# Performance work log

Hardware: AMD Instinct MI355X
Metric: run time of the kernel (lower is better)

The kernel has to match this reference:

```python
import math
import jax, jax.numpy as jnp
from jax import lax
import numpy as np

BSZ, NQ, L, DM, DI, H, HD, DDIST, DCONV, DHID = 2, 128, 2048, 256, 512, 8, 64, 16, 4, 64
DKEY = DI * 2 + 2 + H  # key_proj output: z + xbc + per-head dt bias
DCV = DI + 2           # depthwise conv channels


def setup_inputs() -> dict:
    key = jax.random.key(0)
    ks = jax.random.split(key, 40)
    it = iter(range(40))
    def n(shape, s=1.0):
        return jax.random.normal(ks[next(it)], shape, jnp.float32) * s
    # dt_bias init exactly as in torch module
    dt = jnp.exp(jax.random.uniform(ks[next(it)], (H,)) * (math.log(0.1) - math.log(0.001)) + math.log(0.001))
    dt = jnp.maximum(dt, 1e-4)
    dt_bias = dt + jnp.log(-jnp.expm1(-dt))
    A_log = jnp.log(jax.random.uniform(ks[next(it)], (H,), minval=1.0, maxval=16.0))
    return {
        'queries': n((BSZ, NQ, DM)), 'anchors': n((BSZ, NQ, 3), 10.0),
        'features_perm': n((BSZ, L, DM)), 'pos_embed_perm': n((BSZ, L, DM)),
        'key_pos_3d': n((BSZ, L, 3), 10.0), 'query_pos': n((BSZ, NQ, DM)),
        'key_proj_w': n((DM, DKEY), 0.02),
        'key_conv_w': n((DCV, DCONV), 0.1), 'key_conv_b': jnp.zeros((DCV,)),
        'query_proj_w': n((DM, DI), 0.02),
        'dist_w1': n((3, DHID), 0.3), 'dist_b1': jnp.zeros((DHID,)), 'dist_w2': n((DHID, DDIST), 0.1),
        'bc_proj_w': n((DDIST, 2), 0.2), 'dt_proj_w': n((DDIST, H), 0.2),
        'dt_bias': dt_bias, 'A_log': A_log, 'D': jnp.ones((H,)),
        'key_norm_w': jnp.ones((DI,)), 'out_key_proj_w': n((DI, DM), 0.02),
        'query_norm_w': jnp.ones((DI,)), 'query_norm_b': jnp.zeros((DI,)),
        'out_query_proj_w': n((DI, DM), 0.02),
        'ffn_norm_w': jnp.ones((DM,)), 'ffn_norm_b': jnp.zeros((DM,)),
        'ffn_fc1_w': n((DM, 8 * DM), 0.02), 'ffn_fc1_b': jnp.zeros((8 * DM,)),
        'ffn_fc2_w': n((4 * DM, DM), 0.02), 'ffn_fc2_b': jnp.zeros((DM,)),
    }


def _ln(x, w, b, eps=1e-5):
    m = jnp.mean(x, -1, keepdims=True)
    v = jnp.mean((x - m) ** 2, -1, keepdims=True)
    return (x - m) * lax.rsqrt(v + eps) * w + b


def _dwconv_causal(x, w, b):
    # x [B,L,C], w [C,K]; torch pads K-1 both sides then slices [:L] == causal left pad
    lhs = jnp.swapaxes(x, 1, 2)  # [B,C,L]
    out = lax.conv_general_dilated(lhs, w[:, None, :], (1,), [(DCONV - 1, 0)],
                                   feature_group_count=w.shape[0],
                                   dimension_numbers=('NCH', 'OIH', 'NCH'))
    return jnp.swapaxes(out + b[None, :, None], 1, 2)


def _issm(x, dt, A, Bs, Cs, Dp, init):
    # x [B,L,H,P]; dt [B,L,H,N]; A [H,N]; Bs/Cs [B,L,N]; init [B,H,P,N]
    def step(h, inp):
        xt, dtt, bt, ct = inp  # [B,H,P], [B,H,N], [B,N], [B,N]
        h = h * jnp.exp(dtt * A)[:, :, None, :] + (dtt * bt[:, None, :])[:, :, None, :] * xt[..., None]
        return h, jnp.einsum('bhpn,bn->bhp', h, ct)
    xs = (jnp.swapaxes(x, 0, 1), jnp.swapaxes(dt, 0, 1), jnp.swapaxes(Bs, 0, 1), jnp.swapaxes(Cs, 0, 1))
    h_last, ys = lax.scan(step, init, xs)
    y = jnp.swapaxes(ys, 0, 1) + x * Dp[None, None, :, None]  # D skip inside scan, as in ISSM_chunk_scan_combined
    return y, h_last


def _forward(queries, anchors, features_perm, pos_embed_perm, key_pos_3d, query_pos,
             key_proj_w, key_conv_w, key_conv_b, query_proj_w, dist_w1, dist_b1, dist_w2,
             bc_proj_w, dt_proj_w, dt_bias, A_log, D, key_norm_w, out_key_proj_w,
             query_norm_w, query_norm_b, out_query_proj_w, ffn_norm_w, ffn_norm_b,
             ffn_fc1_w, ffn_fc1_b, ffn_fc2_w, ffn_fc2_b):
    qp = queries + query_pos
    kp = (features_perm + pos_embed_perm) @ key_proj_w            # [B,L,DKEY]
    z, xbc, dtb_seq = kp[..., :DI], kp[..., DI:DI + DCV], kp[..., DI + DCV:]
    xbc = jax.nn.silu(_dwconv_causal(xbc, key_conv_w, key_conv_b))
    x = xbc[..., :DI]
    b_bias, c_bias = xbc[..., DI], xbc[..., DI + 1]               # [B,L]
    init = (qp @ query_proj_w).reshape(BSZ, NQ, H, HD).transpose(0, 2, 3, 1)  # [B,H,HD,NQ]
    # distance features: delta [B,L,NQ,3]
    delta = anchors[:, None, :, :] - key_pos_3d[:, :, None, :]
    enc = jnp.sign(delta) * jnp.log2(jnp.abs(delta) * 20.0 + 1.0) / math.log2(8.0) / 4.0
    feat = jax.nn.relu(enc @ dist_w1 + dist_b1) @ dist_w2         # [B,L,NQ,DDIST]
    bc = feat @ bc_proj_w                                         # [B,L,NQ,2]
    Bssm = bc[..., 0] + b_bias[..., None]                         # [B,L,NQ]
    Cssm = bc[..., 1] + c_bias[..., None]
    dtb = jnp.swapaxes(feat @ dt_proj_w, 2, 3)                    # [B,L,H,NQ]
    dt = jax.nn.softplus(dtb + dtb_seq[..., None] + dt_bias[None, None, :, None])
    A = jnp.broadcast_to(-jnp.exp(A_log)[:, None], (H, NQ))
    xs = x.reshape(BSZ, L, H, HD)
    y_f, h_f = _issm(xs, dt, A, Bssm, Cssm, D, init)
    fl = lambda a: jnp.flip(a, axis=1)
    y_b, h_b = _issm(fl(xs), fl(dt), A, fl(Bssm), fl(Cssm), D, init)
    y = (y_f + fl(y_b)) * 0.5
    h = (h_f + h_b) * 0.5                                         # [B,H,HD,NQ]
    y = y.reshape(BSZ, L, DI) + x * jnp.repeat(D, HD)[None, None, :]
    # gated RMSNorm (norm_before_gate=False): gate first, then normalize
    g = y * jax.nn.silu(z)
    g = g * lax.rsqrt(jnp.mean(g * g, -1, keepdims=True) + 1e-5) * key_norm_w
    out_feat = features_perm + g @ out_key_proj_w
    hs = h.transpose(0, 3, 1, 2).reshape(BSZ, NQ, DI)             # b h hd n -> b n (h hd)
    out_q = queries + _ln(hs, query_norm_w, query_norm_b) @ out_query_proj_w
    fn = _ln(out_q, ffn_norm_w, ffn_norm_b)
    a, v = jnp.split(fn @ ffn_fc1_w + ffn_fc1_b, 2, axis=-1)
    out_q = out_q + (jax.nn.gelu(a, approximate=False) * v) @ ffn_fc2_w + ffn_fc2_b
    return out_q, out_feat


def reference(queries, anchors, features_perm, pos_embed_perm, key_pos_3d, query_pos,
              key_proj_w, key_conv_w, key_conv_b, query_proj_w, dist_w1, dist_b1, dist_w2,
              bc_proj_w, dt_proj_w, dt_bias, A_log, D, key_norm_w, out_key_proj_w,
              query_norm_w, query_norm_b, out_query_proj_w, ffn_norm_w, ffn_norm_b,
              ffn_fc1_w, ffn_fc1_b, ffn_fc2_w, ffn_fc2_b):
    return _forward(queries, anchors, features_perm, pos_embed_perm, key_pos_3d, query_pos,
                    key_proj_w, key_conv_w, key_conv_b, query_proj_w, dist_w1, dist_b1, dist_w2,
                    bc_proj_w, dt_proj_w, dt_bias, A_log, D, key_norm_w, out_key_proj_w,
                    query_norm_w, query_norm_b, out_query_proj_w, ffn_norm_w, ffn_norm_b,
                    ffn_fc1_w, ffn_fc1_b, ffn_fc2_w, ffn_fc2_b)
```

## Files before the change

### kernel.cpp

```cpp
#include <hip/hip_runtime.h>

typedef unsigned short u16;
typedef __bf16 bf16x8 __attribute__((ext_vector_type(8)));
typedef u16 u16x8 __attribute__((ext_vector_type(8)));
typedef float f32x4 __attribute__((ext_vector_type(4)));

#define BSZ_ 2
#define NQ_ 128
#define LSEQ_ 2048
#define DM_ 256
#define DI_ 512
#define NH_ 8
#define HD_ 64
#define DKEY_ 1034
#define DCV_ 514
#define NCHUNK_ 16
#define CT_ 128

__device__ __forceinline__ float bf2f(u16 u) {
  unsigned v = ((unsigned)u) << 16;
  return __builtin_bit_cast(float, v);
}
__device__ __forceinline__ u16 f2bf(float f) {
  unsigned u = __builtin_bit_cast(unsigned, f);
  u += 0x7fffu + ((u >> 16) & 1u);
  return (u16)(u >> 16);
}
__device__ __forceinline__ float sigmoidf_(float x) { return 1.f / (1.f + expf(-x)); }
__device__ __forceinline__ float softplusf_(float x) {
  return (x > 20.f) ? x : log1pf(expf(x));
}

template<bool F32>
__device__ __forceinline__ float ldi(const void* p, size_t i) {
  return F32 ? ((const float*)p)[i] : bf2f(((const u16*)p)[i]);
}
template<bool F32>
__device__ __forceinline__ void sto(void* p, size_t i, float v) {
  if (F32) ((float*)p)[i] = v;
  else ((u16*)p)[i] = f2bf(v);
}

__device__ __forceinline__ bool detect_f32(const void* feat) {
  int lane = threadIdx.x & 63;
  float a = fabsf(bf2f(((const u16*)feat)[2*lane]));
  bool plaus = (a > 1e-6f) && (a < 1e6f);
  unsigned long long m = __ballot(plaus);
  return __popcll(m) < 32;
}

constexpr size_t SZ_KP    = (size_t)BSZ_*LSEQ_*DKEY_;
constexpr size_t SZ_XACT  = (size_t)BSZ_*LSEQ_*DCV_;
constexpr size_t SZ_AW    = (size_t)BSZ_*NH_*LSEQ_*NQ_*2;
constexpr size_t SZ_CARR  = (size_t)BSZ_*LSEQ_*NQ_;
constexpr size_t SZ_QPROJ = (size_t)BSZ_*NQ_*DI_;
constexpr size_t SZ_YACC  = (size_t)BSZ_*LSEQ_*DI_;
constexpr size_t SZ_SEND  = (size_t)BSZ_*NH_*2*NCHUNK_*NQ_*HD_;
constexpr size_t SZ_PTOT  = (size_t)BSZ_*NH_*2*NCHUNK_*NQ_;
constexpr size_t SZ_H0    = SZ_SEND;
constexpr size_t SZ_HB    = (size_t)BSZ_*NH_*2*NQ_*HD_;
constexpr size_t SZ_GBUF  = (size_t)BSZ_*LSEQ_*DI_/2;
constexpr size_t SZ_OUTQF = (size_t)BSZ_*NQ_*DM_;
constexpr size_t SZ_WPREP = 2048;

constexpr size_t OFF_KP    = 0;
constexpr size_t OFF_XACT  = OFF_KP + SZ_KP;
constexpr size_t OFF_AW    = OFF_XACT + SZ_XACT;
constexpr size_t OFF_CARR  = OFF_AW + SZ_AW;
constexpr size_t OFF_QPROJ = OFF_CARR + SZ_CARR;
constexpr size_t OFF_YACC  = OFF_QPROJ + SZ_QPROJ;
constexpr size_t OFF_SEND  = OFF_YACC + SZ_YACC;
constexpr size_t OFF_PTOT  = OFF_SEND + SZ_SEND;
constexpr size_t OFF_H0    = OFF_PTOT + SZ_PTOT;
constexpr size_t OFF_HB    = OFF_H0 + SZ_H0;
constexpr size_t OFF_GBUF  = OFF_HB + SZ_HB;
constexpr size_t OFF_OUTQF = OFF_GBUF + SZ_GBUF;
constexpr size_t OFF_WPREP = OFF_OUTQF + SZ_OUTQF;
constexpr size_t WS_FLOATS = OFF_WPREP + SZ_WPREP;

constexpr size_t OFF_UG  = OFF_AW;
constexpr size_t OFF_LNQ = OFF_UG + (size_t)256*1024/2;
constexpr size_t OFF_LNF = OFF_LNQ + (size_t)256*512/2;

constexpr size_t OFF_ABUF = OFF_SEND;
constexpr size_t OFF_AQ   = OFF_ABUF + (size_t)4096*256/2;
constexpr size_t OFF_BKEY = OFF_AQ + (size_t)256*256/2;
constexpr size_t OFF_BQ   = OFF_BKEY + (size_t)(256*1034+1)/2 + 1;
constexpr size_t OFF_BOK  = OFF_SEND;
constexpr size_t OFF_BOQ  = OFF_BOK + (size_t)512*256/2;
constexpr size_t OFF_B1W  = OFF_BOQ + (size_t)512*256/2;
constexpr size_t OFF_B2W  = OFF_B1W + (size_t)256*2048/2;

template<bool F32>
__device__ void prep_body(const void* A_log, const void* dt_bias,
                          const void* w1, const void* b1, const void* w2,
                          const void* bcw, const void* dtw, float* wp) {
  int t = threadIdx.x;
  if (t < 8) {
    wp[t]     = -expf(ldi<F32>(A_log, t));
    wp[8 + t] = ldi<F32>(dt_bias, t);
  }
  if (t < 64) {
    wp[32 + t*4 + 0] = ldi<F32>(w1, 0*64 + t);
    wp[32 + t*4 + 1] = ldi<F32>(w1, 1*64 + t);
    wp[32 + t*4 + 2] = ldi<F32>(w1, 2*64 + t);
    wp[32 + t*4 + 3] = ldi<F32>(b1, t);
  }
  for (int i = t; i < 1024; i += 256) wp[288 + i] = ldi<F32>(w2, i);
  if (t < 32)  wp[1312 + t] = ldi<F32>(bcw, t);
  if (t < 128) wp[1344 + t] = ldi<F32>(dtw, t);
}

__device__ __forceinline__ void cast_job(bool F32, const void* s0, const void* s1_,
                                         u16* d, size_t n, size_t base, size_t stride) {
  for (size_t i = base; i < n; i += stride) {
    float v = F32 ? ((const float*)s0)[i] : bf2f(((const u16*)s0)[i]);
    if (s1_) v += F32 ? ((const float*)s1_)[i] : bf2f(((const u16*)s1_)[i]);
    d[i] = f2bf(v);
  }
}

__global__ __launch_bounds__(256) void setup_kernel(
    const void* feat, const void* pe, u16* abuf,
    const void* q, const void* qp, u16* aq,
    const void* kw, u16* bkey, const void* qw, u16* bq,
    const void* A_log, const void* dt_bias, const void* w1, const void* b1,
    const void* w2, const void* bcw, const void* dtw, float* wp,
    float* yacc, int* flag)
{
  int bx = blockIdx.x, tid = threadIdx.x;
  if (bx < 512) {
    size_t base = (size_t)bx * 4096 + tid;
#pragma unroll
    for (int k = 0; k < 16; ++k) yacc[base + (size_t)k*256] = 0.f;
    return;
  }
  bool F32 = detect_f32(feat);
  if (bx < 1024) {
    cast_job(F32, feat, pe, abuf, (size_t)4096*256,
             (size_t)(bx-512)*256 + tid, (size_t)512*256);
  } else if (bx < 1056) {
    cast_job(F32, q, qp, aq, (size_t)256*256,
             (size_t)(bx-1024)*256 + tid, (size_t)32*256);
  } else if (bx < 1184) {
    cast_job(F32, kw, nullptr, bkey, (size_t)256*1034,
             (size_t)(bx-1056)*256 + tid, (size_t)128*256);
  } else if (bx < 1248) {
    cast_job(F32, qw, nullptr, bq, (size_t)256*512,
             (size_t)(bx-1184)*256 + tid, (size_t)64*256);
  } else {
    if (tid == 0) *flag = F32 ? 1 : 0;
    if (F32) prep_body<true>(A_log, dt_bias, w1, b1, w2, bcw, dtw, wp);
    else     prep_body<false>(A_log, dt_bias, w1, b1, w2, bcw, dtw, wp);
  }
}

template<int A_MODE, int B_MODE, int OUT_EXT, int RES_EXT, int RES_F32, int BIAS, bool F32>
__device__ void gemm_body(int bm, int bn,
                          const void* A0, const void* A1, const void* Bw,
                          float* Cf, void* Cext, const void* ResE,
                          const float* ResF, const void* Bias,
                          int M, int N, int K) {
  __shared__ u16 As[64][40];
  __shared__ u16 Bs[64][42];
  int tid = threadIdx.x;
  int w = tid >> 6, lane = tid & 63;
  f32x4 acc[4];
#pragma unroll
  for (int j = 0; j < 4; ++j) acc[j] = (f32x4){0.f, 0.f, 0.f, 0.f};

  int arow = tid >> 2, aseg = (tid & 3) * 8;
  int bkl = tid >> 3, bns = (tid & 7) * 8;

  for (int k0 = 0; k0 < K; k0 += 32) {
    {
      size_t abase = (size_t)(bm + arow) * K + k0 + aseg;
      u16x8 tv;
      if (A_MODE == 0) {
#pragma unroll
        for (int i = 0; i < 8; ++i)
          tv[i] = f2bf(ldi<F32>(A0, abase + i) + ldi<F32>(A1, abase + i));
      } else {
        const u16* pa = (const u16*)A0 + abase;
#pragma unroll
        for (int i = 0; i < 8; ++i) tv[i] = pa[i];
      }
      *(u16x8*)&As[arow][aseg] = tv;
    }
    {
      size_t bbase = (size_t)(k0 + bkl) * N + bn + bns;
#pragma unroll
      for (int i = 0; i < 8; ++i) {
        u16 v;
        if (bn + bns + i < N) {
          if (B_MODE == 1) v = ((const u16*)Bw)[bbase + i];
          else             v = f2bf(ldi<F32>(Bw, bbase + i));
        } else v = (u16)0;
        Bs[bns + i][bkl] = v;
      }
    }
    __syncthreads();
    int mrow = w * 16 + (lane & 15);
    int kq = (lane >> 4) * 8;
    bf16x8 af = __builtin_bit_cast(bf16x8, *(const u16x8*)&As[mrow][kq]);
#pragma unroll
    for (int j = 0; j < 4; ++j) {
      bf16x8 bfv = __builtin_bit_cast(bf16x8, *(const u16x8*)&Bs[j*16 + (lane & 15)][kq]);
      acc[j] = __builtin_amdgcn_mfma_f32_16x16x32_bf16(af, bfv, acc[j], 0, 0, 0);
    }
    __syncthreads();
  }
  int col0 = lane & 15, rbase = (lane >> 4) * 4;
#pragma unroll
  for (int j = 0; j < 4; ++j) {
#pragma unroll
    for (int r = 0; r < 4; ++r) {
      int row = bm + w * 16 + rbase + r;
      int col = bn + j * 16 + col0;
      if (col < N) {
        size_t idx = (size_t)row * N + col;
        float v = acc[j][r];
        if (BIAS)    v += ldi<F32>(Bias, col);
        if (RES_EXT) v += ldi<F32>(ResE, idx);
        if (RES_F32) v += ResF[idx];
        if (OUT_EXT) sto<F32>(Cext, idx, v);
        else         Cf[idx] = v;
      }
    }
  }
}

__global__ __launch_bounds__(256) void kp_gemm_kernel(
    const u16* abuf, const u16* bkey, float* kp) {
  gemm_body<1,1,0,0,0,0,false>(blockIdx.x*64, blockIdx.y*64, abuf, nullptr, bkey,
                               kp, nullptr, nullptr, nullptr, nullptr,
                               4096, DKEY_, DM_);
}

template<bool F32>
__device__ void fc2_body(const u16* ug, const u16* b2w, void* out_q,
                         const float* outqf, const void* b2) {
  gemm_body<1,1,1,0,1,1,F32>((blockIdx.x&3)*64, (blockIdx.x>>2)*64, ug, nullptr,
                             b2w, nullptr, out_q, nullptr, outqf, b2,
                             BSZ_*NQ_, DM_, 1024);
}
__global__ __launch_bounds__(256) void fc2_kernel(
    const int* fl, const u16* ug, const u16* b2w, void* out_q,
    const float* outqf, const void* b2) {
  if (*fl) fc2_body<true>(ug, b2w, out_q, outqf, b2);
  else     fc2_body<false>(ug, b2w, out_q, outqf, b2);
}

template<bool F32>
__device__ void conv_body(const float* kp, const void* cw, const void* cb,
                          float* xact) {
  int row = blockIdx.x;
  int l = row & (LSEQ_ - 1);
  for (int ch = threadIdx.x; ch < DCV_; ch += 256) {
    float acc = ldi<F32>(cb, ch);
#pragma unroll
    for (int k = 0; k < 4; ++k) {
      int ll = l - 3 + k;
      if (ll >= 0)
        acc = fmaf(ldi<F32>(cw, ch*4 + k), kp[(size_t)(row - 3 + k)*DKEY_ + DI_ + ch], acc);
    }
    xact[(size_t)row*DCV_ + ch] = acc * sigmoidf_(acc);
  }
}
__global__ __launch_bounds__(256) void convqp_kernel(
    const int* fl, const float* kp, const void* cw, const void* cb, float* xact,
    const u16* aq, const u16* bq, float* qproj)
{
  int bx = blockIdx.x;
  if (bx < 4096) {
    if (*fl) conv_body<true>(kp, cw, cb, xact);
    else     conv_body<false>(kp, cw, cb, xact);
  } else {
    int i = bx - 4096;
    gemm_body<1,1,0,0,0,0,false>((i&3)*64, (i>>2)*64, aq, nullptr, bq,
                                 qproj, nullptr, nullptr, nullptr, nullptr,
                                 BSZ_*NQ_, DI_, DM_);
  }
}

template<bool F32>
__device__ void dist_body(const void* anchors, const void* key_pos,
                          const float* kp, const float* xact, const float* wp,
                          float* aw, float* carr) {
  int tid = threadIdx.x;
  int n = tid & 127;
  int idx = blockIdx.x;
  int b = idx >> 10;
  int l = ((idx & 1023) << 1) | (tid >> 7);
  size_t row = (size_t)b * LSEQ_ + l;

  float enc0, enc1, enc2;
  {
    float e[3];
#pragma unroll
    for (int d = 0; d < 3; ++d) {
      float delta = ldi<F32>(anchors, (b*NQ_ + n)*3 + d) - ldi<F32>(key_pos, row*3 + d);
      float s = delta < 0.f ? -1.f : 1.f;
      e[d] = s * log2f(fabsf(delta) * 20.f + 1.f) * (1.f/12.f);
    }
    enc0 = e[0]; enc1 = e[1]; enc2 = e[2];
  }
  float feat[16];
#pragma unroll
  for (int f = 0; f < 16; ++f) feat[f] = 0.f;
  for (int j = 0; j < 64; ++j) {
    float w0 = wp[32 + j*4], w1v = wp[33 + j*4], w2v = wp[34 + j*4], bb = wp[35 + j*4];
    float hj = fmaxf(fmaf(enc0, w0, fmaf(enc1, w1v, fmaf(enc2, w2v, bb))), 0.f);
#pragma unroll
    for (int f = 0; f < 16; ++f) feat[f] = fmaf(hj, wp[288 + j*16 + f], feat[f]);
  }
  float bc0 = 0.f, bc1 = 0.f;
#pragma unroll
  for (int f = 0; f < 16; ++f) {
    bc0 = fmaf(feat[f], wp[1312 + f*2], bc0);
    bc1 = fmaf(feat[f], wp[1313 + f*2], bc1);
  }
  float bb_ = xact[row*DCV_ + DI_];
  float cb_ = xact[row*DCV_ + DI_ + 1];
  float Bs = bc0 + bb_, Cs = bc1 + cb_;
  carr[row*NQ_ + n] = Cs;

  float dtb[8];
#pragma unroll
  for (int h = 0; h < 8; ++h) dtb[h] = 0.f;
#pragma unroll
  for (int f = 0; f < 16; ++f)
#pragma unroll
    for (int h = 0; h < 8; ++h) dtb[h] = fmaf(feat[f], wp[1344 + f*8 + h], dtb[h]);

#pragma unroll
  for (int h = 0; h < 8; ++h) {
    float xln = dtb[h] + kp[row*DKEY_ + (DI_*2 + 2) + h] + wp[8 + h];
    float dtv = softplusf_(xln);
    float a = expf(dtv * wp[h]);
    float wv = dtv * Bs;
    size_t o = (((size_t)(b*NH_ + h)*LSEQ_ + l)*NQ_ + n)*2;
    aw[o] = a;
    aw[o + 1] = wv;
  }
}
__global__ __launch_bounds__(256) void dist_kernel(
    const int* fl, const void* anchors, const void* key_pos, const float* kp,
    const float* xact, const float* wp, float* aw, float* carr) {
  if (*fl) dist_body<true>(anchors, key_pos, kp, xact, wp, aw, carr);
  else     dist_body<false>(anchors, key_pos, kp, xact, wp, aw, carr);
}

__global__ __launch_bounds__(256) void s1m_kernel(
    const float* __restrict__ aw, const float* __restrict__ xact,
    float* __restrict__ send, float* __restrict__ ptot)
{
  int tid = threadIdx.x;
  int hd = tid & 63;
  int w = __builtin_amdgcn_readfirstlane(tid >> 6);
  int ns = blockIdx.x, q = blockIdx.y, z = blockIdx.z;
  int h = z & 7, b = z >> 3;
  int n0 = __builtin_amdgcn_readfirstlane(ns*16 + w*4);

  float hf[4], hb[4], pr[4];
#pragma unroll
  for (int i = 0; i < 4; ++i) { hf[i] = 0.f; hb[i] = 0.f; pr[i] = 1.f; }

  size_t awbase = (size_t)z * LSEQ_ * (NQ_*2);
  int t = q*CT_;
  for (int s = 0; s < CT_; ++s, ++t) {
    const float* awt = aw + awbase + (size_t)t*(NQ_*2) + n0*2;
    float xv = xact[((size_t)(b*LSEQ_ + t))*DCV_ + (h << 6) + hd];
#pragma unroll
    for (int i = 0; i < 4; ++i) {
      float a = awt[2*i], wv = awt[2*i + 1];
      float wx = wv * xv;
      hf[i] = fmaf(hf[i], a, wx);
      hb[i] = fmaf(pr[i], wx, hb[i]);
      pr[i] *= a;
    }
  }
  size_t cbf = (size_t)((z*2 + 0)*NCHUNK_ + q);
  size_t cbb = (size_t)((z*2 + 1)*NCHUNK_ + (NCHUNK_ - 1 - q));
#pragma unroll
  for (int i = 0; i < 4; ++i) {
    send[cbf*(NQ_*HD_) + (size_t)(n0 + i)*HD_ + hd] = hf[i];
    send[cbb*(NQ_*HD_) + (size_t)(n0 + i)*HD_ + hd] = hb[i];
  }
  if (hd == 0) {
#pragma unroll
    for (int i = 0; i < 4; ++i) {
      ptot[cbf*NQ_ + n0 + i] = pr[i];
      ptot[cbb*NQ_ + n0 + i] = pr[i];
    }
  }
}

__global__ __launch_bounds__(256) void s2_kernel(
    const float* __restrict__ qproj, const float* __restrict__ ptot,
    const float* __restrict__ send, float* __restrict__ h0buf,
    float* __restrict__ hbuf)
{
  int g = blockIdx.x*256 + threadIdx.x;
  int hd = g & 63;
  int n = (g >> 6) & 127;
  int dir = (g >> 13) & 1;
  int h = (g >> 14) & 7;
  int b = g >> 17;
  float hcur = qproj[((size_t)(b*NQ_ + n))*DI_ + h*HD_ + hd];
  size_t base = (size_t)((b*NH_ + h)*2 + dir) * NCHUNK_;
  for (int q = 0; q < NCHUNK_; ++q) {
    size_t cb = base + q;
    h0buf[cb*(NQ_*HD_) + (size_t)n*HD_ + hd] = hcur;
    hcur = fmaf(hcur, ptot[cb*NQ_ + n], send[cb*(NQ_*HD_) + (size_t)n*HD_ + hd]);
  }
  hbuf[((size_t)((b*NH_ + h)*2 + dir))*(NQ_*HD_) + (size_t)n*HD_ + hd] = hcur;
}

template<bool F32>
__device__ void cast1_part(const void* okw, u16* bok, const void* oqw, u16* boq,
                           const void* w1, u16* b1w, const void* w2, u16* b2w) {
  int i = blockIdx.x - 2048;
  int job = i >> 7, bj = i & 127;
  size_t base = (size_t)bj*256 + threadIdx.x, stride = (size_t)128*256;
  switch (job) {
    case 0: cast_job(F32, okw, nullptr, bok, (size_t)512*256, base, stride); break;
    case 1: cast_job(F32, oqw, nullptr, boq, (size_t)512*256, base, stride); break;
    case 2: cast_job(F32, w1, nullptr, b1w, (size_t)256*2048, base, stride); break;
    default: cast_job(F32, w2, nullptr, b2w, (size_t)1024*256, base, stride); break;
  }
}
__global__ __launch_bounds__(256) void s3cast_kernel(
    const int* fl, const float* __restrict__ aw, const float* __restrict__ carr,
    const float* __restrict__ xact, const float* __restrict__ h0buf,
    float* __restrict__ yacc,
    const void* okw, u16* bok, const void* oqw, u16* boq,
    const void* w1, u16* b1w, const void* w2, u16* b2w)
{
  int bx = blockIdx.x;
  if (bx >= 2048) {
    if (*fl) cast1_part<true>(okw, bok, oqw, boq, w1, b1w, w2, b2w);
    else     cast1_part<false>(okw, bok, oqw, boq, w1, b1w, w2, b2w);
    return;
  }
  int tid = threadIdx.x;
  int hd = tid & 63;
  int w = __builtin_amdgcn_readfirstlane(tid >> 6);
  int ns = bx & 3, q = (bx >> 2) & 15, zz = bx >> 6;
  int dir = zz & 1, h = (zz >> 1) & 7, b = zz >> 4;
  int z = b*NH_ + h;
  int n0 = __builtin_amdgcn_readfirstlane(ns*32 + w*8);

  float hst[8];
  size_t cb = (size_t)(((b*NH_ + h)*2 + dir)*NCHUNK_ + q);
#pragma unroll
  for (int i = 0; i < 8; ++i)
    hst[i] = h0buf[cb*(NQ_*HD_) + (size_t)(n0 + i)*HD_ + hd];

  __shared__ float ybuf[2][4][64];
  size_t awbase = (size_t)z * LSEQ_ * (NQ_*2);
  int tbase = dir ? (LSEQ_ - 1 - q*CT_) : (q*CT_);
  int tstep = dir ? -1 : 1;
  const float* awt = aw + awbase + (size_t)tbase*(NQ_*2) + n0*2;
  const float* ct  = carr + ((size_t)(b*LSEQ_) + tbase)*NQ_ + n0;
  const float* xa  = xact + ((size_t)(b*LSEQ_) + tbase)*DCV_ + (h << 6) + hd;
  long awstep = (long)tstep * (NQ_*2);
  long ctstep = (long)tstep * NQ_;
  long xastep = (long)tstep * DCV_;
  float* yrow = yacc + ((size_t)(b*LSEQ_) + tbase)*DI_ + (h << 6) + hd;
  long ystep = (long)tstep * DI_;

  int p = 0;
  for (int s = 0; s < CT_; ++s) {
    float xv = *xa;
    float ys = 0.f;
#pragma unroll
    for (int i = 0; i < 8; ++i) {
      hst[i] = fmaf(hst[i], awt[2*i], awt[2*i + 1] * xv);
      ys = fmaf(hst[i], ct[i], ys);
    }
    ybuf[p][w][hd] = ys;
    asm volatile("s_waitcnt lgkmcnt(0)" ::: "memory");
    __builtin_amdgcn_s_barrier();
    if (w == (s & 3)) {
      float yv = ybuf[p][0][hd] + ybuf[p][1][hd]
               + ybuf[p][2][hd] + ybuf[p][3][hd];
      atomicAdd(yrow, 0.5f * yv);
    }
    yrow += ystep;
    awt += awstep; ct += ctstep; xa += xastep;
    p ^= 1;
  }
}

__device__ __forceinline__ float block_sum256(float v, float* red) {
#pragma unroll
  for (int off = 32; off; off >>= 1) v += __shfl_xor(v, off, 64);
  int wv = threadIdx.x >> 6;
  if ((threadIdx.x & 63) == 0) red[wv] = v;
  __syncthreads();
  float t = red[0] + red[1] + red[2] + red[3];
  __syncthreads();
  return t;
}

template<bool F32>
__device__ void g_body(const float* yacc, const float* xact, const float* kp,
                       const void* Dv, const void* knw, u16* gbuf) {
  int row = blockIdx.x, tid = threadIdx.x;
  __shared__ float red[4];
  float gg[2];
  float ss = 0.f;
#pragma unroll
  for (int ii = 0; ii < 2; ++ii) {
    int ch = tid + ii*256;
    float yv = yacc[(size_t)row*DI_ + ch];
    float xv = xact[(size_t)row*DCV_ + ch];
    float zv = kp[(size_t)row*DKEY_ + ch];
    float Dh = ldi<F32>(Dv, ch >> 6);
    float yf = yv + 2.f * Dh * xv;
    float g = yf * (zv * sigmoidf_(zv));
    gg[ii] = g;
    ss += g * g;
  }
  float tot = block_sum256(ss, red);
  float r = rsqrtf(tot / (float)DI_ + 1e-5f);
#pragma unroll
  for (int ii = 0; ii < 2; ++ii) {
    int ch = tid + ii*256;
    gbuf[(size_t)row*DI_ + ch] = f2bf(gg[ii] * r * ldi<F32>(knw, ch));
  }
}
template<bool F32>
__device__ void lnq_body(const float* hbuf, const void* qnw, const void* qnb,
                         u16* lnq) {
  int row = blockIdx.x - 4096;
  int b = row >> 7, n = row & 127;
  int tid = threadIdx.x;
  __shared__ float red[4];
  float hv[2];
  float s1 = 0.f, s2 = 0.f;
#pragma unroll
  for (int ii = 0; ii < 2; ++ii) {
    int ch = tid + ii*256;
    int h = ch >> 6, hd = ch & 63;
    size_t base = ((size_t)((b*NH_ + h)*2))*(NQ_*HD_) + (size_t)n*HD_ + hd;
    float v = 0.5f * (hbuf[base] + hbuf[base + (size_t)NQ_*HD_]);
    hv[ii] = v;
    s1 += v;
    s2 += v * v;
  }
  s1 = block_sum256(s1, red);
  s2 = block_sum256(s2, red);
  float mean = s1 / (float)DI_;
  float var = fmaxf(s2 / (float)DI_ - mean * mean, 0.f);
  float rstd = rsqrtf(var + 1e-5f);
#pragma unroll
  for (int ii = 0; ii < 2; ++ii) {
    int ch = tid + ii*256;
    lnq[(size_t)row*DI_ + ch] =
        f2bf((hv[ii] - mean) * rstd * ldi<F32>(qnw, ch) + ldi<F32>(qnb, ch));
  }
}
__global__ __launch_bounds__(256) void glnq_kernel(
    const int* fl, const float* yacc, const float* xact, const float* kp,
    const void* Dv, const void* knw, u16* gbuf,
    const float* hbuf, const void* qnw, const void* qnb, u16* lnq)
{
  if (blockIdx.x < 4096) {
    if (*fl) g_body<true>(yacc, xact, kp, Dv, knw, gbuf);
    else     g_body<false>(yacc, xact, kp, Dv, knw, gbuf);
  } else {
    if (*fl) lnq_body<true>(hbuf, qnw, qnb, lnq);
    else     lnq_body<false>(hbuf, qnw, qnb, lnq);
  }
}

template<bool F32>
__device__ void ofoq_body(const u16* gbuf, const u16* bok, void* out_feat,
                          const void* features, const u16* lnq, const u16* boq,
                          float* outqf, const void* queries) {
  int bx = blockIdx.x;
  if (bx < 256) {
    gemm_body<1,1,1,1,0,0,F32>((bx>>2)*64, (bx&3)*64, gbuf, nullptr, bok,
                               nullptr, out_feat, features, nullptr, nullptr,
                               4096, DM_, DI_);
  } else {
    int i = bx - 256;
    gemm_body<1,1,0,1,0,0,F32>((i&3)*64, (i>>2)*64, lnq, nullptr, boq,
                               outqf, nullptr, queries, nullptr, nullptr,
                               BSZ_*NQ_, DM_, DI_);
  }
}
__global__ __launch_bounds__(256) void ofoq_kernel(
    const int* fl, const u16* gbuf, const u16* bok,
    void* out_feat_f32, void* out_feat_bf16, const void* features,
    const u16* lnq, const u16* boq, float* outqf, const void* queries) {
  if (*fl) ofoq_body<true>(gbuf, bok, out_feat_f32, features, lnq, boq, outqf, queries);
  else     ofoq_body<false>(gbuf, bok, out_feat_bf16, features, lnq, boq, outqf, queries);
}

template<bool F32>
__device__ void lnf_body(const float* outqf, const void* fnw, const void* fnb,
                         u16* lnf) {
  int row = blockIdx.x, tid = threadIdx.x;
  __shared__ float red[4];
  float x = outqf[(size_t)row*DM_ + tid];
  float s1 = block_sum256(x, red);
  float s2 = block_sum256(x * x, red);
  float mean = s1 / (float)DM_;
  float var = fmaxf(s2 / (float)DM_ - mean * mean, 0.f);
  float rstd = rsqrtf(var + 1e-5f);
  lnf[(size_t)row*DM_ + tid] =
      f2bf((x - mean) * rstd * ldi<F32>(fnw, tid) + ldi<F32>(fnb, tid));
}
__global__ __launch_bounds__(256) void lnf_kernel(
    const int* fl, const float* outqf, const void* fnw, const void* fnb, u16* lnf) {
  if (*fl) lnf_body<true>(outqf, fnw, fnb, lnf);
  else     lnf_body<false>(outqf, fnw, fnb, lnf);
}

template<bool F32>
__device__ void fc1g_body(const u16* lnf, const u16* b1w, const void* b1, u16* ug) {
  __shared__ u16 As[64][40];
  __shared__ u16 BsA[64][42];
  __shared__ u16 BsV[64][42];
  int tid = threadIdx.x;
  int w = tid >> 6, lane = tid & 63;
  int bm = blockIdx.x * 64, bn = blockIdx.y * 64;
  f32x4 accA[4], accV[4];
#pragma unroll
  for (int j = 0; j < 4; ++j) {
    accA[j] = (f32x4){0.f, 0.f, 0.f, 0.f};
    accV[j] = (f32x4){0.f, 0.f, 0.f, 0.f};
  }
  int arow = tid >> 2, aseg = (tid & 3) * 8;
  int bkl = tid >> 3, bns = (tid & 7) * 8;

  for (int k0 = 0; k0 < DM_; k0 += 32) {
    {
      size_t abase = (size_t)(bm + arow) * DM_ + k0 + aseg;
      const u16* pa = lnf + abase;
      u16x8 tv;
#pragma unroll
      for (int i = 0; i < 8; ++i) tv[i] = pa[i];
      *(u16x8*)&As[arow][aseg] = tv;
    }
    {
      size_t bbase = (size_t)(k0 + bkl) * 2048 + bn + bns;
#pragma unroll
      for (int i = 0; i < 8; ++i) {
        BsA[bns + i][bkl] = b1w[bbase + i];
        BsV[bns + i][bkl] = b1w[bbase + 1024 + i];
      }
    }
    __syncthreads();
    int mrow = w * 16 + (lane & 15);
    int kq = (lane >> 4) * 8;
    bf16x8 af = __builtin_bit_cast(bf16x8, *(const u16x8*)&As[mrow][kq]);
#pragma unroll
    for (int j = 0; j < 4; ++j) {
      bf16x8 ba = __builtin_bit_cast(bf16x8, *(const u16x8*)&BsA[j*16 + (lane & 15)][kq]);
      bf16x8 bv = __builtin_bit_cast(bf16x8, *(const u16x8*)&BsV[j*16 + (lane & 15)][kq]);
      accA[j] = __builtin_amdgcn_mfma_f32_16x16x32_bf16(af, ba, accA[j], 0, 0, 0);
      accV[j] = __builtin_amdgcn_mfma_f32_16x16x32_bf16(af, bv, accV[j], 0, 0, 0);
    }
    __syncthreads();
  }
  int col0 = lane & 15, rbase = (lane >> 4) * 4;
#pragma unroll
  for (int j = 0; j < 4; ++j) {
#pragma unroll
    for (int r = 0; r < 4; ++r) {
      int row = bm + w * 16 + rbase + r;
      int col = bn + j * 16 + col0;
      float a = accA[j][r] + ldi<F32>(b1, col);
      float v = accV[j][r] + ldi<F32>(b1, col + 1024);
      float ge = 0.5f * a * (1.f + erff(a * 0.70710678118f));
      ug[(size_t)row*1024 + col] = f2bf(ge * v);
    }
  }
}
__global__ __launch_bounds__(256) void fc1g_kernel(
    const int* fl, const u16* lnf, const u16* b1w, const void* b1, u16* ug) {
  if (*fl) fc1g_body<true>(lnf, b1w, b1, ug);
  else     fc1g_body<false>(lnf, b1w, b1, ug);
}

extern "C" void kernel_launch(void* const* d_in, const int* in_sizes, int n_in,
                              void* d_out, int out_size, void* d_ws, size_t ws_size,
                              hipStream_t stream) {
  const void* queries        = d_in[0];
  const void* anchors        = d_in[1];
  const void* features       = d_in[2];
  const void* pos_embed      = d_in[3];
  const void* key_pos        = d_in[4];
  const void* query_pos      = d_in[5];
  const void* key_proj_w     = d_in[6];
  const void* key_conv_w     = d_in[7];
  const void* key_conv_b     = d_in[8];
  const void* query_proj_w   = d_in[9];
  const void* dist_w1        = d_in[10];
  const void* dist_b1        = d_in[11];
  const void* dist_w2        = d_in[12];
  const void* bc_proj_w      = d_in[13];
  const void* dt_proj_w      = d_in[14];
  const void* dt_bias        = d_in[15];
  const void* A_log          = d_in[16];
  const void* Dvec           = d_in[17];
  const void* key_norm_w     = d_in[18];
  const void* out_key_proj_w = d_in[19];
  const void* query_norm_w   = d_in[20];
  const void* query_norm_b   = d_in[21];
  const void* out_query_proj_w = d_in[22];
  const void* ffn_norm_w     = d_in[23];
  const void* ffn_norm_b     = d_in[24];
  const void* ffn_fc1_w      = d_in[25];
  const void* ffn_fc1_b      = d_in[26];
  const void* ffn_fc2_w      = d_in[27];
  const void* ffn_fc2_b      = d_in[28];

  if (ws_size < WS_FLOATS * sizeof(float)) return;

  float* ws    = (float*)d_ws;
  float* kp    = ws + OFF_KP;
  float* xact  = ws + OFF_XACT;
  float* aw    = ws + OFF_AW;
  float* carr  = ws + OFF_CARR;
  float* qproj = ws + OFF_QPROJ;
  float* yacc  = ws + OFF_YACC;
  float* send  = ws + OFF_SEND;
  float* ptot  = ws + OFF_PTOT;
  float* h0buf = ws + OFF_H0;
  float* hbuf  = ws + OFF_HB;
  u16*   gbuf  = (u16*)(ws + OFF_GBUF);
  float* outqf = ws + OFF_OUTQF;
  float* wprep = ws + OFF_WPREP;
  int*   flag  = (int*)(wprep + 1536);
  u16*   ugbuf = (u16*)(ws + OFF_UG);
  u16*   lnq   = (u16*)(ws + OFF_LNQ);
  u16*   lnf   = (u16*)(ws + OFF_LNF);
  u16*   abuf  = (u16*)(ws + OFF_ABUF);
  u16*   aq    = (u16*)(ws + OFF_AQ);
  u16*   bkey  = (u16*)(ws + OFF_BKEY);
  u16*   bq    = (u16*)(ws + OFF_BQ);
  u16*   bok   = (u16*)(ws + OFF_BOK);
  u16*   boq   = (u16*)(ws + OFF_BOQ);
  u16*   b1w   = (u16*)(ws + OFF_B1W);
  u16*   b2w   = (u16*)(ws + OFF_B2W);

  void* out_q = d_out;
  void* out_feat_bf16 = (void*)((u16*)d_out + (size_t)BSZ_*NQ_*DM_);
  void* out_feat_f32  = (void*)((float*)d_out + (size_t)BSZ_*NQ_*DM_);

  setup_kernel<<<1249, 256, 0, stream>>>(
      features, pos_embed, abuf, queries, query_pos, aq,
      key_proj_w, bkey, query_proj_w, bq,
      A_log, dt_bias, dist_w1, dist_b1, dist_w2, bc_proj_w, dt_proj_w, wprep,
      yacc, flag);

  kp_gemm_kernel<<<dim3(64, 17), 256, 0, stream>>>(abuf, bkey, kp);

  convqp_kernel<<<4096 + 32, 256, 0, stream>>>(
      flag, kp, key_conv_w, key_conv_b, xact, aq, bq, qproj);

  dist_kernel<<<BSZ_*LSEQ_/2, 256, 0, stream>>>(flag, anchors, key_pos, kp, xact,
                                                wprep, aw, carr);

  s1m_kernel<<<dim3(8, NCHUNK_, BSZ_*NH_), 256, 0, stream>>>(aw, xact, send, ptot);

  s2_kernel<<<1024, 256, 0, stream>>>(qproj, ptot, send, h0buf, hbuf);

  s3cast_kernel<<<2048 + 512, 256, 0, stream>>>(
      flag, aw, carr, xact, h0buf, yacc,
      out_key_proj_w, bok, out_query_proj_w, boq, ffn_fc1_w, b1w, ffn_fc2_w, b2w);

  glnq_kernel<<<4096 + 256, 256, 0, stream>>>(
      flag, yacc, xact, kp, Dvec, key_norm_w, gbuf,
      hbuf, query_norm_w, query_norm_b, lnq);

  ofoq_kernel<<<256 + 16, 256, 0, stream>>>(
      flag, gbuf, bok, out_feat_f32, out_feat_bf16, features,
      lnq, boq, outqf, queries);

  lnf_kernel<<<BSZ_*NQ_, 256, 0, stream>>>(flag, outqf, ffn_norm_w, ffn_norm_b, lnf);

  fc1g_kernel<<<dim3(4, 16), 256, 0, stream>>>(flag, lnf, b1w, ffn_fc1_b, ugbuf);

  fc2_kernel<<<16, 256, 0, stream>>>(flag, ugbuf, b2w, out_q, outqf, ffn_fc2_b);
}
```

Before: 443.4 us.

## Batch scan barriers over eight timesteps and double-buffer vector coefficient loads

Restructures the chunked selective-scan loop so each workgroup barrier and LDS reduction covers eight timesteps instead of one. The per-state coefficient pairs are now loaded as float4 vectors into two alternating register sets, so the next step's loads are issued before the current step computes. The y dot product is split into two accumulators to shorten the dependency chain. The cost is more registers and a larger LDS buffer, and the atomic adds from one wave come in bursts of eight.

```diff
diff --git a/kernel.cpp b/kernel.cpp
--- a/kernel.cpp
+++ b/kernel.cpp
@@ -451,46 +451,81 @@
   int z = b*NH_ + h;
   int n0 = __builtin_amdgcn_readfirstlane(ns*32 + w*8);
 
-  float hst[8];
-  size_t cb = (size_t)(((b*NH_ + h)*2 + dir)*NCHUNK_ + q);
-#pragma unroll
-  for (int i = 0; i < 8; ++i)
-    hst[i] = h0buf[cb*(NQ_*HD_) + (size_t)(n0 + i)*HD_ + hd];
-
-  __shared__ float ybuf[2][4][64];
-  size_t awbase = (size_t)z * LSEQ_ * (NQ_*2);
+  float h0_, h1_, h2_, h3_, h4_, h5_, h6_, h7_;
+  {
+    size_t cb = (size_t)((z*2 + dir)*NCHUNK_ + q);
+    const float* hp = h0buf + cb*(NQ_*HD_) + (size_t)n0*HD_ + hd;
+    h0_ = hp[0*HD_]; h1_ = hp[1*HD_]; h2_ = hp[2*HD_]; h3_ = hp[3*HD_];
+    h4_ = hp[4*HD_]; h5_ = hp[5*HD_]; h6_ = hp[6*HD_]; h7_ = hp[7*HD_];
+  }
+
+  __shared__ float ybuf[2][8][4][64];
   int tbase = dir ? (LSEQ_ - 1 - q*CT_) : (q*CT_);
   int tstep = dir ? -1 : 1;
-  const float* awt = aw + awbase + (size_t)tbase*(NQ_*2) + n0*2;
-  const float* ct  = carr + ((size_t)(b*LSEQ_) + tbase)*NQ_ + n0;
-  const float* xa  = xact + ((size_t)(b*LSEQ_) + tbase)*DCV_ + (h << 6) + hd;
+  const float* __restrict__ awt = aw + (size_t)z*LSEQ_*(NQ_*2)
+                                  + (size_t)tbase*(NQ_*2) + n0*2;
+  const float* __restrict__ ct  = carr + ((size_t)(b*LSEQ_) + tbase)*NQ_ + n0;
+  const float* __restrict__ xa  = xact + ((size_t)(b*LSEQ_) + tbase)*DCV_
+                                  + (h << 6) + hd;
   long awstep = (long)tstep * (NQ_*2);
   long ctstep = (long)tstep * NQ_;
   long xastep = (long)tstep * DCV_;
   float* yrow = yacc + ((size_t)(b*LSEQ_) + tbase)*DI_ + (h << 6) + hd;
   long ystep = (long)tstep * DI_;
 
+  float ys0, ys1, ys2, ys3, ys4, ys5, ys6, ys7;
+  f32x4 Aa0, Aa1, Aa2, Aa3;
+  f32x4 Ba0, Ba1, Ba2, Ba3;
+
+#define PREFS(X) {                                                    \
+    X##a0 = *(const f32x4*)(awt);     X##a1 = *(const f32x4*)(awt+4); \
+    X##a2 = *(const f32x4*)(awt+8);   X##a3 = *(const f32x4*)(awt+12);\
+    awt += awstep; }
+
+#define COMPS(X, YS) {                                                \
+    float xv = *xa;                                                   \
+    float ya, yb;                                                     \
+    h0_ = fmaf(h0_, X##a0[0], X##a0[1]*xv); ya = h0_ * ct[0];         \
+    h1_ = fmaf(h1_, X##a0[2], X##a0[3]*xv); yb = h1_ * ct[1];         \
+    h2_ = fmaf(h2_, X##a1[0], X##a1[1]*xv); ya = fmaf(h2_, ct[2], ya);\
+    h3_ = fmaf(h3_, X##a1[2], X##a1[3]*xv); yb = fmaf(h3_, ct[3], yb);\
+    h4_ = fmaf(h4_, X##a2[0], X##a2[1]*xv); ya = fmaf(h4_, ct[4], ya);\
+    h5_ = fmaf(h5_, X##a2[2], X##a2[3]*xv); yb = fmaf(h5_, ct[5], yb);\
+    h6_ = fmaf(h6_, X##a3[0], X##a3[1]*xv); ya = fmaf(h6_, ct[6], ya);\
+    h7_ = fmaf(h7_, X##a3[2], X##a3[3]*xv); yb = fmaf(h7_, ct[7], yb);\
+    YS = ya + yb;                                                     \
+    ct += ctstep; xa += xastep; }
+
+  PREFS(A);
   int p = 0;
-  for (int s = 0; s < CT_; ++s) {
-    float xv = *xa;
-    float ys = 0.f;
-#pragma unroll
-    for (int i = 0; i < 8; ++i) {
-      hst[i] = fmaf(hst[i], awt[2*i], awt[2*i + 1] * xv);
-      ys = fmaf(hst[i], ct[i], ys);
-    }
-    ybuf[p][w][hd] = ys;
+  for (int g = 0; g < 16; ++g) {
+    PREFS(B); COMPS(A, ys0);
+    PREFS(A); COMPS(B, ys1);
+    PREFS(B); COMPS(A, ys2);
+    PREFS(A); COMPS(B, ys3);
+    PREFS(B); COMPS(A, ys4);
+    PREFS(A); COMPS(B, ys5);
+    PREFS(B); COMPS(A, ys6);
+    PREFS(A); COMPS(B, ys7);
+    ybuf[p][0][w][hd] = ys0;  ybuf[p][1][w][hd] = ys1;
+    ybuf[p][2][w][hd] = ys2;  ybuf[p][3][w][hd] = ys3;
+    ybuf[p][4][w][hd] = ys4;  ybuf[p][5][w][hd] = ys5;
+    ybuf[p][6][w][hd] = ys6;  ybuf[p][7][w][hd] = ys7;
     asm volatile("s_waitcnt lgkmcnt(0)" ::: "memory");
     __builtin_amdgcn_s_barrier();
-    if (w == (s & 3)) {
-      float yv = ybuf[p][0][hd] + ybuf[p][1][hd]
-               + ybuf[p][2][hd] + ybuf[p][3][hd];
-      atomicAdd(yrow, 0.5f * yv);
-    }
-    yrow += ystep;
-    awt += awstep; ct += ctstep; xa += xastep;
+    if (w == (g & 3)) {
+#pragma unroll
+      for (int k = 0; k < 8; ++k) {
+        float yv = ybuf[p][k][0][hd] + ybuf[p][k][1][hd]
+                 + ybuf[p][k][2][hd] + ybuf[p][k][3][hd];
+        atomicAdd(yrow + (long)k*ystep, 0.5f * yv);
+      }
+    }
+    yrow += 8L*ystep;
     p ^= 1;
   }
+#undef PREFS
+#undef COMPS
 }
 
 __device__ __forceinline__ float block_sum256(float v, float* red) {
```

New measurement: 451.7 us. About the same (+1.9%).

## Stage scan coefficients in LDS with double-buffered 8-step prefetch

Applied to the files above, without the earlier changes.

Rewrites the chunked scan loop so each block cooperatively loads 8 timesteps of decay/input coefficients, C values and x activations into double-buffered shared memory, prefetching the next group into registers while computing the current one. Per-step partial outputs are collected in LDS and reduced and atomically added once per 8-step group, spread across waves. This replaces per-thread scattered global loads and a barrier every timestep with coalesced vector loads and two barriers per 8 steps. It costs more shared memory per block and adds register pressure for the prefetch.

```diff
diff --git a/kernel.cpp b/kernel.cpp
--- a/kernel.cpp
+++ b/kernel.cpp
@@ -4,6 +4,7 @@
 typedef __bf16 bf16x8 __attribute__((ext_vector_type(8)));
 typedef u16 u16x8 __attribute__((ext_vector_type(8)));
 typedef float f32x4 __attribute__((ext_vector_type(4)));
+typedef float f32x2 __attribute__((ext_vector_type(2)));
 
 #define BSZ_ 2
 #define NQ_ 128
@@ -443,53 +444,99 @@
     else     cast1_part<false>(okw, bok, oqw, boq, w1, b1w, w2, b2w);
     return;
   }
+  __shared__ float awl[2][8][64];
+  __shared__ float ctl[2][8][32];
+  __shared__ float xl [2][8][64];
+  __shared__ float yl [8][4][64];
+
   int tid = threadIdx.x;
   int hd = tid & 63;
   int w = __builtin_amdgcn_readfirstlane(tid >> 6);
   int ns = bx & 3, q = (bx >> 2) & 15, zz = bx >> 6;
   int dir = zz & 1, h = (zz >> 1) & 7, b = zz >> 4;
   int z = b*NH_ + h;
-  int n0 = __builtin_amdgcn_readfirstlane(ns*32 + w*8);
-
-  float hst[8];
-  size_t cb = (size_t)(((b*NH_ + h)*2 + dir)*NCHUNK_ + q);
-#pragma unroll
-  for (int i = 0; i < 8; ++i)
-    hst[i] = h0buf[cb*(NQ_*HD_) + (size_t)(n0 + i)*HD_ + hd];
-
-  __shared__ float ybuf[2][4][64];
-  size_t awbase = (size_t)z * LSEQ_ * (NQ_*2);
+  int n0 = ns*32 + w*8;
+
   int tbase = dir ? (LSEQ_ - 1 - q*CT_) : (q*CT_);
   int tstep = dir ? -1 : 1;
-  const float* awt = aw + awbase + (size_t)tbase*(NQ_*2) + n0*2;
-  const float* ct  = carr + ((size_t)(b*LSEQ_) + tbase)*NQ_ + n0;
-  const float* xa  = xact + ((size_t)(b*LSEQ_) + tbase)*DCV_ + (h << 6) + hd;
-  long awstep = (long)tstep * (NQ_*2);
-  long ctstep = (long)tstep * NQ_;
-  long xastep = (long)tstep * DCV_;
+
+  int s8 = tid >> 5, j = tid & 31;
+  const float* awg = aw + (size_t)z*LSEQ_*(NQ_*2)
+                     + (size_t)(tbase + tstep*s8)*(NQ_*2) + ns*64 + j*2;
+  const float* ctg = carr + ((size_t)(b*LSEQ_) + tbase + tstep*s8)*NQ_ + ns*32 + j;
+  const float* xg  = xact + ((size_t)(b*LSEQ_) + tbase + tstep*s8)*DCV_ + (h<<6) + j*2;
+  long awgstep = (long)tstep*8*(NQ_*2);
+  long ctgstep = (long)tstep*8*NQ_;
+  long xgstep  = (long)tstep*8*DCV_;
+
+  f32x2 pa = *(const f32x2*)awg;
+  float pc = *ctg;
+  f32x2 px = *(const f32x2*)xg;
+  awg += awgstep; ctg += ctgstep; xg += xgstep;
+
+  float h0_, h1_, h2_, h3_, h4_, h5_, h6_, h7_;
+  {
+    size_t cb = (size_t)((z*2 + dir)*NCHUNK_ + q);
+    const float* hp = h0buf + cb*(NQ_*HD_) + (size_t)n0*HD_ + hd;
+    h0_ = hp[0*HD_]; h1_ = hp[1*HD_]; h2_ = hp[2*HD_]; h3_ = hp[3*HD_];
+    h4_ = hp[4*HD_]; h5_ = hp[5*HD_]; h6_ = hp[6*HD_]; h7_ = hp[7*HD_];
+  }
+  *(f32x2*)&awl[0][s8][j*2] = pa;
+  ctl[0][s8][j] = pc;
+  *(f32x2*)&xl[0][s8][j*2] = px;
+  asm volatile("s_waitcnt lgkmcnt(0)" ::: "memory");
+  __builtin_amdgcn_s_barrier();
+
   float* yrow = yacc + ((size_t)(b*LSEQ_) + tbase)*DI_ + (h << 6) + hd;
   long ystep = (long)tstep * DI_;
 
   int p = 0;
-  for (int s = 0; s < CT_; ++s) {
-    float xv = *xa;
-    float ys = 0.f;
-#pragma unroll
-    for (int i = 0; i < 8; ++i) {
-      hst[i] = fmaf(hst[i], awt[2*i], awt[2*i + 1] * xv);
-      ys = fmaf(hst[i], ct[i], ys);
-    }
-    ybuf[p][w][hd] = ys;
+  f32x2 sa; float sc; f32x2 sx;
+  for (int g = 0; g < 16; ++g) {
+    if (g < 15) {
+      sa = *(const f32x2*)awg; sc = *ctg; sx = *(const f32x2*)xg;
+      awg += awgstep; ctg += ctgstep; xg += xgstep;
+    }
+    if (g > 0) {
+#pragma unroll
+      for (int r = 0; r < 2; ++r) {
+        int s = w + r*4;
+        float yv = yl[s][0][hd] + yl[s][1][hd] + yl[s][2][hd] + yl[s][3][hd];
+        atomicAdd(yrow + (long)((g-1)*8 + s)*ystep, 0.5f * yv);
+      }
+    }
     asm volatile("s_waitcnt lgkmcnt(0)" ::: "memory");
     __builtin_amdgcn_s_barrier();
-    if (w == (s & 3)) {
-      float yv = ybuf[p][0][hd] + ybuf[p][1][hd]
-               + ybuf[p][2][hd] + ybuf[p][3][hd];
-      atomicAdd(yrow, 0.5f * yv);
-    }
-    yrow += ystep;
-    awt += awstep; ct += ctstep; xa += xastep;
+#pragma unroll
+    for (int s = 0; s < 8; ++s) {
+      const float* A = &awl[p][s][w*16];
+      const float* C = &ctl[p][s][w*8];
+      float xv = xl[p][s][hd];
+      float ya, yb;
+      h0_ = fmaf(h0_, A[0],  A[1]*xv);  ya = h0_ * C[0];
+      h1_ = fmaf(h1_, A[2],  A[3]*xv);  yb = h1_ * C[1];
+      h2_ = fmaf(h2_, A[4],  A[5]*xv);  ya = fmaf(h2_, C[2], ya);
+      h3_ = fmaf(h3_, A[6],  A[7]*xv);  yb = fmaf(h3_, C[3], yb);
+      h4_ = fmaf(h4_, A[8],  A[9]*xv);  ya = fmaf(h4_, C[4], ya);
+      h5_ = fmaf(h5_, A[10], A[11]*xv); yb = fmaf(h5_, C[5], yb);
+      h6_ = fmaf(h6_, A[12], A[13]*xv); ya = fmaf(h6_, C[6], ya);
+      h7_ = fmaf(h7_, A[14], A[15]*xv); yb = fmaf(h7_, C[7], yb);
+      yl[s][w][hd] = ya + yb;
+    }
+    if (g < 15) {
+      *(f32x2*)&awl[p^1][s8][j*2] = sa;
+      ctl[p^1][s8][j] = sc;
+      *(f32x2*)&xl[p^1][s8][j*2] = sx;
+    }
+    asm volatile("s_waitcnt lgkmcnt(0)" ::: "memory");
+    __builtin_amdgcn_s_barrier();
     p ^= 1;
+  }
+#pragma unroll
+  for (int r = 0; r < 2; ++r) {
+    int s = w + r*4;
+    float yv = yl[s][0][hd] + yl[s][1][hd] + yl[s][2][hd] + yl[s][3][hd];
+    atomicAdd(yrow + (long)(15*8 + s)*ystep, 0.5f * yv);
   }
 }
 
```

Result: faster. 422.6 us (-4.7%).
